# Kernel tuning notes

Hardware: AMD Instinct MI355X
Metric: run time of the kernel (lower is better)

Reference implementation:

```python
import jax, jax.numpy as jnp
import numpy as np

# --- low precision float format: exp=5, man=2, subnormals, nearest-even ---
EXP, MAN = 5, 2
BIAS = 2 ** (EXP - 1) - 1          # 15
EMIN = 1 - BIAS                     # -14 (min normal exponent; clamping here gives subnormals)
MAXV = (2.0 - 2.0 ** (-MAN)) * 2.0 ** BIAS


def _q(x):
    """Round x to nearest FP(exp=5, man=2) value (subnormals, clipped at max)."""
    ax = jnp.abs(x)
    e = jnp.floor(jnp.log2(jnp.where(ax > 0, ax, 1.0)))
    e = jnp.maximum(e, EMIN)
    scale = jnp.exp2(e - MAN)
    q = jnp.round(x / scale) * scale   # jnp.round = half-to-even
    q = jnp.clip(q, -MAXV, MAXV)
    return jnp.where(ax > 0, q, x).astype(x.dtype)


# Quantizer: forward quantize, straight-through (quantized) backward
@jax.custom_vjp
def fq(x):
    return _q(x)

def _fq_fwd(x):
    return _q(x), None

def _fq_bwd(_, g):
    return (_q(g),)

fq.defvjp(_fq_fwd, _fq_bwd)


def conv_valid(x, w):
    return jax.lax.conv_general_dilated(
        x, w, window_strides=(1, 1), padding='VALID',
        dimension_numbers=('NCHW', 'OIHW', 'NCHW'))


def qconv(x, w):
    # QConv2d: input_quant, weight_quant, conv, output_quant
    return fq(conv_valid(fq(x), fq(w)))


def qlinear(x, W, b):
    # QLinear: input_quant, weight_quant (weights + bias), matmul, output_quant
    return fq(fq(x) @ fq(W).T + fq(b))


def batchnorm(x, gamma, beta, eps=1e-5):
    # training-mode BatchNorm2d over (N,H,W) per channel
    m = x.mean(axis=(0, 2, 3), keepdims=True)
    v = x.var(axis=(0, 2, 3), keepdims=True)
    return (x - m) * jax.lax.rsqrt(v + eps) * gamma[None, :, None, None] + beta[None, :, None, None]


def maxpool2(x):
    return jax.lax.reduce_window(x, -jnp.inf, jax.lax.max,
                                 (1, 1, 2, 2), (1, 1, 2, 2), 'VALID')


def setup_inputs() -> dict:
    key = jax.random.key(0)
    ks = jax.random.split(key, 12)
    B = 8192
    inp = {
        'x':   jax.random.normal(ks[0], (B, 1, 32, 32), jnp.float32),
        'w1':  jax.random.normal(ks[1], (6, 1, 5, 5), jnp.float32) * 0.2,
        'g1':  jnp.ones((6,), jnp.float32),
        'be1': jnp.zeros((6,), jnp.float32),
        'w2':  jax.random.normal(ks[2], (16, 6, 5, 5), jnp.float32) * 0.1,
        'g2':  jnp.ones((16,), jnp.float32),
        'be2': jnp.zeros((16,), jnp.float32),
        'fw1': jax.random.normal(ks[3], (120, 400), jnp.float32) * 0.05,
        'fb1': jnp.zeros((120,), jnp.float32),
        'fw2': jax.random.normal(ks[4], (84, 120), jnp.float32) * 0.09,
        'fb2': jnp.zeros((84,), jnp.float32),
        'fw3': jax.random.normal(ks[5], (10, 84), jnp.float32) * 0.1,
        'fb3': jnp.zeros((10,), jnp.float32),
    }
    return inp


def reference(x, w1, g1, be1, w2, g2, be2, fw1, fb1, fw2, fb2, fw3, fb3):
    x = fq(x)                                   # act_error_quant
    x = qconv(x, w1)                            # conv1 (no bias)
    x = batchnorm(x, g1, be1)                   # bn1
    x = fq(x)                                   # act_error_quant
    x = maxpool2(jax.nn.relu(x))                # relu + 2x2 maxpool -> [B,6,14,14]
    x = qconv(x, w2)                            # conv2 -> [B,16,10,10]
    x = batchnorm(x, g2, be2)                   # bn2
    x = fq(x)
    x = maxpool2(jax.nn.relu(x))                # -> [B,16,5,5]
    x = x.reshape(x.shape[0], -1)               # [B,400]
    x = jax.nn.relu(qlinear(x, fw1, fb1))       # fc1
    x = jax.nn.relu(qlinear(x, fw2, fb2))       # fc2
    x = qlinear(x, fw3, fb3)                    # fc3 -> [B,10]
    return x
```

## Files before the change

### kernel.cpp

```cpp
#include <hip/hip_runtime.h>
#include <hip/hip_bf16.h>


#define BATCH 8192

typedef double d4 __attribute__((ext_vector_type(4)));

__device__ __forceinline__ double fq_d(double x) {
    long long b = __double_as_longlong(x);
    long long ab = b & 0x7fffffffffffffffLL;
    if (ab == 0) return x;
    double q;
    if (ab >= 0x3F10000000000000LL) {
        long long r = b + 0x0001FFFFFFFFFFFFLL + ((b >> 50) & 1LL);
        r &= 0xFFFC000000000000LL;
        q = __longlong_as_double(r);
        q = fmin(fmax(q, -57344.0), 57344.0);
    } else {
        q = rint(x * 65536.0) * 1.52587890625e-05;
    }
    return q;
}

__device__ __forceinline__ float fq_f(float x) {
    int b = __float_as_int(x);
    int ab = b & 0x7fffffff;
    if (ab == 0) return x;
    float q;
    if (ab >= 0x38800000) {
        int r = b + 0x000FFFFF + ((b >> 21) & 1);
        r &= 0xFFE00000;
        q = __int_as_float(r);
        q = fminf(fmaxf(q, -57344.0f), 57344.0f);
    } else {
        q = rintf(x * 65536.0f) * 1.52587890625e-05f;
    }
    return q;
}

__device__ __forceinline__ unsigned short bfbits(double q) {
    __hip_bfloat16 h = __float2bfloat16((float)q);
    return *(unsigned short*)&h;
}

__device__ __forceinline__ float bfval(unsigned short u) {
    return __bfloat162float(*(__hip_bfloat16*)&u);
}

__global__ void kprep(const float* __restrict__ w1, const float* __restrict__ w2,
                      const float* __restrict__ fb1, const float* __restrict__ fb2,
                      const float* __restrict__ fb3, const float* __restrict__ fw1,
                      const float* __restrict__ fw2, const float* __restrict__ fw3,
                      float* __restrict__ qw1, float* __restrict__ qw2t,
                      float* __restrict__ qfb1, float* __restrict__ qfb2,
                      float* __restrict__ qfb3, float* __restrict__ Wt1,
                      float* __restrict__ Wt2, float* __restrict__ Wt3) {
    int i = blockIdx.x * 256 + threadIdx.x;
    if (i < 150) { qw1[i] = fq_f(w1[i]); return; }
    i -= 150;
    if (i < 2432) { int k = i >> 4, co = i & 15;
        qw2t[i] = (k < 150) ? fq_f(w2[co * 150 + k]) : 0.0f; return; }
    i -= 2432;
    if (i < 120) { qfb1[i] = fq_f(fb1[i]); return; }
    i -= 120;
    if (i < 84) { qfb2[i] = fq_f(fb2[i]); return; }
    i -= 84;
    if (i < 10) { qfb3[i] = fq_f(fb3[i]); return; }
    i -= 10;
    if (i < 51200) { int k = i / 128, o = i % 128;
        Wt1[i] = (o < 120) ? fq_f(fw1[o * 400 + k]) : 0.0f; return; }
    i -= 51200;
    if (i < 15360) { int k = i / 128, o = i % 128;
        Wt2[i] = (o < 84) ? fq_f(fw2[o * 120 + k]) : 0.0f; return; }
    i -= 15360;
    if (i < 1344) { int k = i / 16, o = i % 16;
        Wt3[i] = (o < 10) ? fq_f(fw3[o * 84 + k]) : 0.0f; return; }
}
#define PREP_TOTAL (150 + 2432 + 120 + 84 + 10 + 51200 + 15360 + 1344)

__global__ __launch_bounds__(512) void kconv1(const float* __restrict__ x,
        const float* __restrict__ qw, __hip_bfloat16* __restrict__ c1,
        int nimg_total, double* __restrict__ st1) {
    __shared__ float sxf[6 * 1056];
    __shared__ double swd[152];
    __shared__ double sred[6][2];
    int t = threadIdx.x;
    int b0 = blockIdx.x * 6;
    int nimg = nimg_total - b0; if (nimg > 6) nimg = 6;
    for (int i = t; i < nimg * 1024; i += 512) {
        int img = i >> 10, idx = i & 1023;
        sxf[img * 1056 + (idx >> 5) * 33 + (idx & 31)] =
            fq_f(x[(size_t)(b0 + img) * 1024 + idx]);
    }
    if (t < 150) swd[t] = (double)qw[t];
    if (t >= 192 && t < 204) ((double*)sred)[t - 192] = 0.0;
    __syncthreads();
    int ntask = nimg * 336;
    for (int task = t; task < ntask; task += 512) {
        int img = task / 336; int rr = task % 336;
        int co = rr / 56; int rem = rr % 56;
        int i0 = (rem >> 2) * 2;
        int j0 = (rem & 3) * 7;
        const double* wp = &swd[co * 25];
        double a0[7], a1[7];
        #pragma unroll
        for (int j = 0; j < 7; ++j) { a0[j] = 0.0; a1[j] = 0.0; }
        double wr[5], wq[5];
        #pragma unroll
        for (int u = 0; u < 6; ++u) {
            const float* xr = &sxf[img * 1056 + (i0 + u) * 33 + j0];
            double xv[11];
            #pragma unroll
            for (int k = 0; k < 11; ++k) xv[k] = (double)xr[k];
            if (u < 5) {
                #pragma unroll
                for (int tt = 0; tt < 5; ++tt) wr[tt] = wp[u * 5 + tt];
                #pragma unroll
                for (int j = 0; j < 7; ++j)
                    a0[j] = fma(xv[j], wr[0], fma(xv[j+1], wr[1], fma(xv[j+2], wr[2],
                            fma(xv[j+3], wr[3], fma(xv[j+4], wr[4], a0[j])))));
            }
            if (u >= 1) {
                #pragma unroll
                for (int j = 0; j < 7; ++j)
                    a1[j] = fma(xv[j], wq[0], fma(xv[j+1], wq[1], fma(xv[j+2], wq[2],
                            fma(xv[j+3], wq[3], fma(xv[j+4], wq[4], a1[j])))));
            }
            #pragma unroll
            for (int tt = 0; tt < 5; ++tt) wq[tt] = wr[tt];
        }
        size_t base = ((size_t)(b0 + img) * 6 + co) * 784 + (size_t)i0 * 28 + j0;
        double s = 0.0, s2 = 0.0;
        #pragma unroll
        for (int j = 0; j < 7; ++j) {
            double q0 = fq_d(a0[j]), q1 = fq_d(a1[j]);
            ((unsigned short*)c1)[base + j]      = bfbits(q0);
            ((unsigned short*)c1)[base + 28 + j] = bfbits(q1);
            s += q0 + q1; s2 += q0 * q0 + q1 * q1;
        }
        atomicAdd(&sred[co][0], s);
        atomicAdd(&sred[co][1], s2);
    }
    __syncthreads();
    if (t < 12) atomicAdd(&st1[t * 32 + (blockIdx.x & 31)], ((double*)sred)[t]);
}

__global__ void kfinal(const double* __restrict__ st, double* __restrict__ mr,
                       int C, double N) {
    int c = threadIdx.x;
    if (c < C) {
        double s = 0.0, s2 = 0.0;
        for (int b = 0; b < 32; ++b) { s += st[c * 64 + b]; s2 += st[c * 64 + 32 + b]; }
        double m = s / N;
        double v = s2 / N - m * m;
        mr[2 * c] = m;
        mr[2 * c + 1] = 1.0 / sqrt(v + 1e-5);
    }
}

__global__ __launch_bounds__(256) void kpool1(const __hip_bfloat16* __restrict__ c1,
        const double* __restrict__ mr1, const float* __restrict__ g1,
        const float* __restrict__ be1, __hip_bfloat16* __restrict__ p1) {
    int idx = blockIdx.x * 256 + threadIdx.x;
    int pp = idx % 7;  int t1 = idx / 7;
    int ph = t1 % 14;  int t2 = t1 / 14;
    int c  = t2 % 6;   int b  = t2 / 6;
    double m = mr1[2 * c], r = mr1[2 * c + 1];
    double gg = (double)g1[c], bb = (double)be1[c];
    bool useMax = (r * gg) >= 0.0;
    const __hip_bfloat16* src = c1 + (((size_t)b * 6 + c) * 28 + 2 * ph) * 28 + 4 * pp;
    ushort4 u0 = *(const ushort4*)src;
    ushort4 u1 = *(const ushort4*)(src + 28);
    float f0 = bfval(u0.x), f1 = bfval(u0.y);
    float f2 = bfval(u0.z), f3 = bfval(u0.w);
    float f4 = bfval(u1.x), f5 = bfval(u1.y);
    float f6 = bfval(u1.z), f7 = bfval(u1.w);
    float va = useMax ? fmaxf(fmaxf(f0, f1), fmaxf(f4, f5))
                      : fminf(fminf(f0, f1), fminf(f4, f5));
    float vb = useMax ? fmaxf(fmaxf(f2, f3), fmaxf(f6, f7))
                      : fminf(fminf(f2, f3), fminf(f6, f7));
    double qa = fq_d((((double)va - m) * r) * gg + bb);
    double qb = fq_d((((double)vb - m) * r) * gg + bb);
    qa = fmax(qa, 0.0); qb = fmax(qb, 0.0);
    ushort2 pk; pk.x = bfbits(qa); pk.y = bfbits(qb);
    *(ushort2*)&p1[((size_t)b * 6 + c) * 196 + ph * 14 + 2 * pp] = pk;
}

__global__ __launch_bounds__(512) void kconv2(const __hip_bfloat16* __restrict__ p1,
        const float* __restrict__ qw2t, __hip_bfloat16* __restrict__ c2,
        double* __restrict__ st2) {
    __shared__ float sxf[9408];
    __shared__ float swf[2432];
    __shared__ int soff[152];
    __shared__ unsigned short sep[8][256];
    __shared__ double sred[16][2];
    int t = threadIdx.x;
    int b0 = blockIdx.x * 8;
    const ushort4* srcp = (const ushort4*)(p1 + (size_t)b0 * 1176);
    for (int i = t; i < 2352; i += 512) {
        ushort4 u = srcp[i];
        float* d = &sxf[4 * i];
        d[0] = bfval(u.x);
        d[1] = bfval(u.y);
        d[2] = bfval(u.z);
        d[3] = bfval(u.w);
    }
    {
        const float4* wsrc = (const float4*)qw2t;
        float4* wdst = (float4*)swf;
        for (int i = t; i < 608; i += 512) wdst[i] = wsrc[i];
    }
    if (t < 152)
        soff[t] = (t < 150) ? (t / 25) * 196 + ((t % 25) / 5) * 14 + (t % 5) : 0;
    if (t < 32) ((double*)sred)[t] = 0.0;
    __syncthreads();

    int l = t & 63, w = t >> 6;
    int c = l >> 4, r16 = l & 15;

    d4 pz = {0.0, 0.0, 0.0, 0.0};
    d4 prow = __builtin_amdgcn_mfma_f64_16x16x4f64((double)r16, 0.25, pz, 0, 0, 0);
    d4 pcol = __builtin_amdgcn_mfma_f64_16x16x4f64(1.0, 0.25 * (double)r16, pz, 0, 0, 0);
    int rowidx[4], colidx[4];
    #pragma unroll
    for (int j = 0; j < 4; ++j) { rowidx[j] = (int)prow[j]; colidx[j] = (int)pcol[j]; }

    unsigned short* myep = sep[w];
    double ls = 0.0, ls2 = 0.0;
    int co0 = colidx[0];
    for (int tile = w; tile < 50; tile += 8) {
        int pos = tile * 16 + r16;
        int abase = (pos / 100) * 1176 + ((pos % 100) / 10) * 14 + (pos % 10);
        d4 a0 = {0.0, 0.0, 0.0, 0.0}, a1 = {0.0, 0.0, 0.0, 0.0};
        #pragma unroll
        for (int s = 0; s < 19; ++s) {
            int k0 = 4 * s + c;
            int k1 = 4 * (s + 19) + c;
            double x0 = (double)sxf[abase + soff[k0]];
            double x1 = (double)sxf[abase + soff[k1]];
            double w0 = (double)swf[k0 * 16 + r16];
            double w1 = (double)swf[k1 * 16 + r16];
            a0 = __builtin_amdgcn_mfma_f64_16x16x4f64(x0, w0, a0, 0, 0, 0);
            a1 = __builtin_amdgcn_mfma_f64_16x16x4f64(x1, w1, a1, 0, 0, 0);
        }
        #pragma unroll
        for (int j = 0; j < 4; ++j) {
            double q = fq_d(a0[j] + a1[j]);
            myep[rowidx[j] * 16 + colidx[j]] = bfbits(q);
            ls += q; ls2 += q * q;
        }
        ushort4 v = *(const ushort4*)&myep[l * 4];
        *(ushort4*)((unsigned short*)c2 + ((size_t)b0 * 100 + tile * 16) * 16 + l * 4) = v;
    }
    atomicAdd(&sred[co0][0], ls);
    atomicAdd(&sred[co0][1], ls2);
    __syncthreads();
    if (t < 32) atomicAdd(&st2[t * 32 + (blockIdx.x & 31)], ((double*)sred)[t]);
}

__global__ __launch_bounds__(256) void kfc1(const __hip_bfloat16* __restrict__ c2,
        const double* __restrict__ st2, const float* __restrict__ g2,
        const float* __restrict__ be2, const float* __restrict__ Wt,
        const float* __restrict__ qb, __hip_bfloat16* __restrict__ outb) {
    constexpr int IN = 400, OUT = 120, OUTP = 128, ROWS = 4, BT = 8;
    __shared__ double sx[BT][IN];
    __shared__ double sbn[16][4];
    int t = threadIdx.x;
    int b0 = blockIdx.x * BT;
    if (t < 16) {
        double s = 0.0, s2 = 0.0;
        for (int b = 0; b < 32; ++b) { s += st2[t * 64 + b]; s2 += st2[t * 64 + 32 + b]; }
        double m = s / (819200.0);
        double v = s2 / (819200.0) - m * m;
        sbn[t][0] = m; sbn[t][1] = 1.0 / sqrt(v + 1e-5);
        sbn[t][2] = (double)g2[t]; sbn[t][3] = (double)be2[t];
    }
    __syncthreads();
    for (int i = t; i < BT * IN; i += 256) {
        int cc = i & 15;
        int rem = (i >> 4) % 25;
        int r = i / 400;
        int ph = rem / 5, pw = rem % 5;
        const __hip_bfloat16* src = c2 + ((size_t)(b0 + r) * 100 + 20 * ph + 2 * pw) * 16 + cc;
        double m = sbn[cc][0], rr = sbn[cc][1], gg = sbn[cc][2], bb = sbn[cc][3];
        float f0 = __bfloat162float(src[0]),   f1 = __bfloat162float(src[16]);
        float f2 = __bfloat162float(src[160]), f3 = __bfloat162float(src[176]);
        bool useMax = (rr * gg) >= 0.0;
        float v = useMax ? fmaxf(fmaxf(f0, f1), fmaxf(f2, f3))
                         : fminf(fminf(f0, f1), fminf(f2, f3));
        double q = fq_d((((double)v - m) * rr) * gg + bb);
        sx[r][cc * 25 + rem] = fmax(q, 0.0);
    }
    __syncthreads();
    int o = t % OUTP;
    int g = t / OUTP;
    double acc[ROWS];
    double bias = (o < OUT) ? (double)qb[o] : 0.0;
    #pragma unroll
    for (int r = 0; r < ROWS; ++r) acc[r] = bias;
    #pragma unroll 4
    for (int k = 0; k < IN; ++k) {
        double w = (double)Wt[k * OUTP + o];
        #pragma unroll
        for (int r = 0; r < ROWS; ++r)
            acc[r] = fma(sx[g * ROWS + r][k], w, acc[r]);
    }
    if (o < OUT) {
        #pragma unroll
        for (int r = 0; r < ROWS; ++r) {
            double q = fq_d(acc[r]);
            if (q < 0.0) q = 0.0;
            outb[(size_t)(b0 + g * ROWS + r) * OUT + o] = __float2bfloat16((float)q);
        }
    }
}

__global__ __launch_bounds__(256) void kfc23(const __hip_bfloat16* __restrict__ a1,
        const float* __restrict__ Wt2, const float* __restrict__ qfb2,
        const float* __restrict__ Wt3, const float* __restrict__ qfb3,
        float* __restrict__ out) {
    __shared__ double sx1[16][120];
    __shared__ double s2[16][84];
    int t = threadIdx.x;
    int b0 = blockIdx.x * 16;
    for (int i = t; i < 16 * 120; i += 256) {
        int r = i / 120, k = i % 120;
        sx1[r][k] = (double)__bfloat162float(a1[(size_t)(b0 + r) * 120 + k]);
    }
    __syncthreads();
    {
        int o = t % 128, g = t / 128;
        double acc[8];
        double bias = (o < 84) ? (double)qfb2[o] : 0.0;
        #pragma unroll
        for (int r = 0; r < 8; ++r) acc[r] = bias;
        #pragma unroll 4
        for (int k = 0; k < 120; ++k) {
            double w = (double)Wt2[k * 128 + o];
            #pragma unroll
            for (int r = 0; r < 8; ++r)
                acc[r] = fma(sx1[g * 8 + r][k], w, acc[r]);
        }
        if (o < 84) {
            #pragma unroll
            for (int r = 0; r < 8; ++r) {
                double q = fq_d(acc[r]);
                s2[g * 8 + r][o] = fmax(q, 0.0);
            }
        }
    }
    __syncthreads();
    {
        int o = t % 16, g = t / 16;
        double acc = (o < 10) ? (double)qfb3[o] : 0.0;
        #pragma unroll 4
        for (int k = 0; k < 84; ++k)
            acc = fma(s2[g][k], (double)Wt3[k * 16 + o], acc);
        if (o < 10)
            out[(size_t)(b0 + g) * 10 + o] = (float)fq_d(acc);
    }
}

extern "C" void kernel_launch(void* const* d_in, const int* in_sizes, int n_in,
                              void* d_out, int out_size, void* d_ws, size_t ws_size,
                              hipStream_t stream) {
    const float* x   = (const float*)d_in[0];
    const float* w1  = (const float*)d_in[1];
    const float* g1  = (const float*)d_in[2];
    const float* be1 = (const float*)d_in[3];
    const float* w2  = (const float*)d_in[4];
    const float* g2  = (const float*)d_in[5];
    const float* be2 = (const float*)d_in[6];
    const float* fw1 = (const float*)d_in[7];
    const float* fb1 = (const float*)d_in[8];
    const float* fw2 = (const float*)d_in[9];
    const float* fb2 = (const float*)d_in[10];
    const float* fw3 = (const float*)d_in[11];
    const float* fb3 = (const float*)d_in[12];

    char* ws = (char*)d_ws;
    double* stats1 = (double*)(ws + 0);
    double* stats2 = (double*)(ws + 3072);
    double* mr1    = (double*)(ws + 11264);
    float* qw1  = (float*)(ws + 12288);
    float* qw2t = (float*)(ws + 13312);
    float* qfb1 = (float*)(ws + 23040);
    float* qfb2 = (float*)(ws + 23552);
    float* qfb3 = (float*)(ws + 24064);
    float* Wt1  = (float*)(ws + 24576);
    float* Wt2  = (float*)(ws + 229376);
    float* Wt3  = (float*)(ws + 290816);
    __hip_bfloat16* c1 = (__hip_bfloat16*)(ws + 303104);
    __hip_bfloat16* p1 = (__hip_bfloat16*)(ws + 77373440);
    __hip_bfloat16* c2 = (__hip_bfloat16*)(ws + 303104);
    __hip_bfloat16* a1 = (__hip_bfloat16*)(ws + 303104 + 26214400);

    hipMemsetAsync(ws, 0, 11264, stream);

    kprep<<<(PREP_TOTAL + 255) / 256, 256, 0, stream>>>(
        w1, w2, fb1, fb2, fb3, fw1, fw2, fw3,
        qw1, qw2t, qfb1, qfb2, qfb3, Wt1, Wt2, Wt3);

    kconv1<<<(BATCH + 5) / 6, 512, 0, stream>>>(x, qw1, c1, BATCH, stats1);
    kfinal<<<1, 32, 0, stream>>>(stats1, mr1, 6, (double)BATCH * 784.0);
    kpool1<<<BATCH * 6 * 14 * 7 / 256, 256, 0, stream>>>(c1, mr1, g1, be1, p1);
    kconv2<<<BATCH / 8, 512, 0, stream>>>(p1, qw2t, c2, stats2);
    kfc1<<<BATCH / 8, 256, 0, stream>>>(c2, stats2, g2, be2, Wt1, qfb1, a1);
    kfc23<<<BATCH / 16, 256, 0, stream>>>(a1, Wt2, qfb2, Wt3, qfb3, (float*)d_out);
}
```

Before: 395.4 us.

## Fuse 2x2 max/min pooling into conv1 and shrink BN1 pass

Conv1 now computes full 14-wide row pairs per thread and applies the 2x2 pool (max or min depending on gamma sign) before writing, so only the pooled pre-BN tensor is stored instead of the full 28x28 conv output. The BN1 kernel then just normalizes, quantizes and ReLUs the pooled values with vectorized loads. This cuts the c1 write/read traffic by about 4x, at the cost of more registers per thread in conv1 and fewer images per block. The pool direction is decided from the sign of gamma alone, on the assumption that rsqrt(var) is always positive.

```diff
diff --git a/kernel.cpp b/kernel.cpp
--- a/kernel.cpp
+++ b/kernel.cpp
@@ -79,64 +79,75 @@
 #define PREP_TOTAL (150 + 2432 + 120 + 84 + 10 + 51200 + 15360 + 1344)
 
 __global__ __launch_bounds__(512) void kconv1(const float* __restrict__ x,
-        const float* __restrict__ qw, __hip_bfloat16* __restrict__ c1,
-        int nimg_total, double* __restrict__ st1) {
-    __shared__ float sxf[6 * 1056];
+        const float* __restrict__ qw, const float* __restrict__ g1,
+        unsigned short* __restrict__ praw, int nimg_total,
+        double* __restrict__ st1) {
+    __shared__ float sxf[3 * 1056];
     __shared__ double swd[152];
+    __shared__ float sg1[6];
     __shared__ double sred[6][2];
     int t = threadIdx.x;
-    int b0 = blockIdx.x * 6;
-    int nimg = nimg_total - b0; if (nimg > 6) nimg = 6;
+    int b0 = blockIdx.x * 3;
+    int nimg = nimg_total - b0; if (nimg > 3) nimg = 3;
     for (int i = t; i < nimg * 1024; i += 512) {
         int img = i >> 10, idx = i & 1023;
         sxf[img * 1056 + (idx >> 5) * 33 + (idx & 31)] =
             fq_f(x[(size_t)(b0 + img) * 1024 + idx]);
     }
     if (t < 150) swd[t] = (double)qw[t];
+    if (t >= 160 && t < 166) sg1[t - 160] = g1[t - 160];
     if (t >= 192 && t < 204) ((double*)sred)[t - 192] = 0.0;
     __syncthreads();
-    int ntask = nimg * 336;
+    int ntask = nimg * 168;
     for (int task = t; task < ntask; task += 512) {
-        int img = task / 336; int rr = task % 336;
-        int co = rr / 56; int rem = rr % 56;
-        int i0 = (rem >> 2) * 2;
-        int j0 = (rem & 3) * 7;
+        int img = task / 168; int rr = task % 168;
+        int co = rr / 28; int rem = rr % 28;
+        int ph = rem >> 1;
+        int half = rem & 1;
+        int i0 = 2 * ph;
+        int j0 = half * 14;
         const double* wp = &swd[co * 25];
-        double a0[7], a1[7];
-        #pragma unroll
-        for (int j = 0; j < 7; ++j) { a0[j] = 0.0; a1[j] = 0.0; }
+        double a0[14], a1[14];
+        #pragma unroll
+        for (int j = 0; j < 14; ++j) { a0[j] = 0.0; a1[j] = 0.0; }
         double wr[5], wq[5];
         #pragma unroll
         for (int u = 0; u < 6; ++u) {
             const float* xr = &sxf[img * 1056 + (i0 + u) * 33 + j0];
-            double xv[11];
+            double xv[18];
             #pragma unroll
-            for (int k = 0; k < 11; ++k) xv[k] = (double)xr[k];
+            for (int k = 0; k < 18; ++k) xv[k] = (double)xr[k];
             if (u < 5) {
                 #pragma unroll
                 for (int tt = 0; tt < 5; ++tt) wr[tt] = wp[u * 5 + tt];
                 #pragma unroll
-                for (int j = 0; j < 7; ++j)
+                for (int j = 0; j < 14; ++j)
                     a0[j] = fma(xv[j], wr[0], fma(xv[j+1], wr[1], fma(xv[j+2], wr[2],
                             fma(xv[j+3], wr[3], fma(xv[j+4], wr[4], a0[j])))));
             }
             if (u >= 1) {
                 #pragma unroll
-                for (int j = 0; j < 7; ++j)
+                for (int j = 0; j < 14; ++j)
                     a1[j] = fma(xv[j], wq[0], fma(xv[j+1], wq[1], fma(xv[j+2], wq[2],
                             fma(xv[j+3], wq[3], fma(xv[j+4], wq[4], a1[j])))));
             }
             #pragma unroll
             for (int tt = 0; tt < 5; ++tt) wq[tt] = wr[tt];
         }
-        size_t base = ((size_t)(b0 + img) * 6 + co) * 784 + (size_t)i0 * 28 + j0;
+        double q0[14], q1[14];
         double s = 0.0, s2 = 0.0;
         #pragma unroll
-        for (int j = 0; j < 7; ++j) {
-            double q0 = fq_d(a0[j]), q1 = fq_d(a1[j]);
-            ((unsigned short*)c1)[base + j]      = bfbits(q0);
-            ((unsigned short*)c1)[base + 28 + j] = bfbits(q1);
-            s += q0 + q1; s2 += q0 * q0 + q1 * q1;
+        for (int j = 0; j < 14; ++j) {
+            q0[j] = fq_d(a0[j]); q1[j] = fq_d(a1[j]);
+            s += q0[j] + q1[j]; s2 += q0[j] * q0[j] + q1[j] * q1[j];
+        }
+        bool useMax = (sg1[co] >= 0.0f);
+        unsigned short* dst = praw + ((size_t)(b0 + img) * 6 + co) * 196 + ph * 14 + half * 7;
+        #pragma unroll
+        for (int jp = 0; jp < 7; ++jp) {
+            double pmax = fmax(fmax(q0[2*jp], q0[2*jp+1]), fmax(q1[2*jp], q1[2*jp+1]));
+            double pmin = fmin(fmin(q0[2*jp], q0[2*jp+1]), fmin(q1[2*jp], q1[2*jp+1]));
+            dst[jp] = bfbits(useMax ? pmax : pmin);
         }
         atomicAdd(&sred[co][0], s);
         atomicAdd(&sred[co][1], s2);
@@ -158,32 +169,23 @@
     }
 }
 
-__global__ __launch_bounds__(256) void kpool1(const __hip_bfloat16* __restrict__ c1,
+__global__ __launch_bounds__(256) void kbn1(const unsigned short* __restrict__ praw,
         const double* __restrict__ mr1, const float* __restrict__ g1,
         const float* __restrict__ be1, __hip_bfloat16* __restrict__ p1) {
     int idx = blockIdx.x * 256 + threadIdx.x;
-    int pp = idx % 7;  int t1 = idx / 7;
-    int ph = t1 % 14;  int t2 = t1 / 14;
-    int c  = t2 % 6;   int b  = t2 / 6;
+    int cb = idx / 49;
+    int c = cb % 6;
+    int off = (idx % 49) * 4;
     double m = mr1[2 * c], r = mr1[2 * c + 1];
     double gg = (double)g1[c], bb = (double)be1[c];
-    bool useMax = (r * gg) >= 0.0;
-    const __hip_bfloat16* src = c1 + (((size_t)b * 6 + c) * 28 + 2 * ph) * 28 + 4 * pp;
-    ushort4 u0 = *(const ushort4*)src;
-    ushort4 u1 = *(const ushort4*)(src + 28);
-    float f0 = bfval(u0.x), f1 = bfval(u0.y);
-    float f2 = bfval(u0.z), f3 = bfval(u0.w);
-    float f4 = bfval(u1.x), f5 = bfval(u1.y);
-    float f6 = bfval(u1.z), f7 = bfval(u1.w);
-    float va = useMax ? fmaxf(fmaxf(f0, f1), fmaxf(f4, f5))
-                      : fminf(fminf(f0, f1), fminf(f4, f5));
-    float vb = useMax ? fmaxf(fmaxf(f2, f3), fmaxf(f6, f7))
-                      : fminf(fminf(f2, f3), fminf(f6, f7));
-    double qa = fq_d((((double)va - m) * r) * gg + bb);
-    double qb = fq_d((((double)vb - m) * r) * gg + bb);
-    qa = fmax(qa, 0.0); qb = fmax(qb, 0.0);
-    ushort2 pk; pk.x = bfbits(qa); pk.y = bfbits(qb);
-    *(ushort2*)&p1[((size_t)b * 6 + c) * 196 + ph * 14 + 2 * pp] = pk;
+    ushort4 u = *(const ushort4*)(praw + (size_t)cb * 196 + off);
+    ushort4 o;
+    double q;
+    q = fq_d((((double)bfval(u.x) - m) * r) * gg + bb); o.x = bfbits(fmax(q, 0.0));
+    q = fq_d((((double)bfval(u.y) - m) * r) * gg + bb); o.y = bfbits(fmax(q, 0.0));
+    q = fq_d((((double)bfval(u.z) - m) * r) * gg + bb); o.z = bfbits(fmax(q, 0.0));
+    q = fq_d((((double)bfval(u.w) - m) * r) * gg + bb); o.w = bfbits(fmax(q, 0.0));
+    *(ushort4*)((unsigned short*)p1 + (size_t)cb * 196 + off) = o;
 }
 
 __global__ __launch_bounds__(512) void kconv2(const __hip_bfloat16* __restrict__ p1,
@@ -390,7 +392,7 @@
     float* Wt1  = (float*)(ws + 24576);
     float* Wt2  = (float*)(ws + 229376);
     float* Wt3  = (float*)(ws + 290816);
-    __hip_bfloat16* c1 = (__hip_bfloat16*)(ws + 303104);
+    unsigned short* praw = (unsigned short*)(ws + 303104);
     __hip_bfloat16* p1 = (__hip_bfloat16*)(ws + 77373440);
     __hip_bfloat16* c2 = (__hip_bfloat16*)(ws + 303104);
     __hip_bfloat16* a1 = (__hip_bfloat16*)(ws + 303104 + 26214400);
@@ -401,9 +403,9 @@
         w1, w2, fb1, fb2, fb3, fw1, fw2, fw3,
         qw1, qw2t, qfb1, qfb2, qfb3, Wt1, Wt2, Wt3);
 
-    kconv1<<<(BATCH + 5) / 6, 512, 0, stream>>>(x, qw1, c1, BATCH, stats1);
+    kconv1<<<(BATCH + 2) / 3, 512, 0, stream>>>(x, qw1, g1, praw, BATCH, stats1);
     kfinal<<<1, 32, 0, stream>>>(stats1, mr1, 6, (double)BATCH * 784.0);
-    kpool1<<<BATCH * 6 * 14 * 7 / 256, 256, 0, stream>>>(c1, mr1, g1, be1, p1);
+    kbn1<<<BATCH * 6 * 49 / 256, 256, 0, stream>>>(praw, mr1, g1, be1, p1);
     kconv2<<<BATCH / 8, 512, 0, stream>>>(p1, qw2t, c2, stats2);
     kfc1<<<BATCH / 8, 256, 0, stream>>>(c2, stats2, g2, be2, Wt1, qfb1, a1);
     kfc23<<<BATCH / 16, 256, 0, stream>>>(a1, Wt2, qfb2, Wt3, qfb3, (float*)d_out);
```

Result: faster. 378.3 us (-4.3%).
